# Performance work log

Measured on AMD Instinct MI355X. Metric: run time of the kernel, lower is better.

## Reference

```python
import jax, jax.numpy as jnp
import numpy as np

THETA = 10000.0
D_K = 128
MAX_SEQ_LEN = 4096
BATCH = 32
SEQ = 4096


def _build_rot(theta, d_k, max_seq_len):
    """Precompute the [max_seq_len, d_k, d_k] block-diagonal 2x2 rotation stack,
    matching the torch module's buffer construction."""
    ks = 2.0 * jnp.arange(d_k // 2, dtype=jnp.float32)
    inv_theta = 1.0 / (theta ** (ks / d_k))                      # [d_k/2]
    pos = jnp.arange(max_seq_len, dtype=jnp.float32)
    ang = pos[:, None] * inv_theta[None, :]                      # [S, d_k/2]
    c, s = jnp.cos(ang), jnp.sin(ang)
    ev = jnp.arange(0, d_k, 2)
    od = ev + 1
    rot = jnp.zeros((max_seq_len, d_k, d_k), dtype=jnp.float32)
    rot = (rot.at[:, ev, ev].set(c)
              .at[:, od, od].set(c)
              .at[:, ev, od].set(-s)
              .at[:, od, ev].set(s))
    return rot


def setup_inputs() -> dict:
    key = jax.random.key(0)
    k1, k2 = jax.random.split(key)
    x = jax.random.normal(k1, (BATCH, SEQ, D_K), dtype=jnp.float32)
    token_positions = jax.random.randint(k2, (BATCH, SEQ), 0, MAX_SEQ_LEN)
    rot = _build_rot(THETA, D_K, MAX_SEQ_LEN)                    # [S, d_k, d_k] buffer
    return {"x": x, "token_positions": token_positions, "rot": rot}


def reference(x, token_positions, rot):
    # The torch forward OVERWRITES token_positions with arange(min_seq_len).
    min_seq_len = min(x.shape[-2], token_positions.shape[-1])
    pos = jnp.arange(min_seq_len)
    # Dense block-diagonal rotation matmul per position (faithful to the module's einsum).
    # rot[pos]: [S, d_k, d_k], x: [B, S, d_k] -> [B, S, d_k]
    return jnp.einsum('sij,bsj->bsi', rot[pos], x)
```

## Files before the change

### kernel.cpp

```cpp
#include <hip/hip_runtime.h>


#define ROPE_DK    128
#define ROPE_HALF  64
#define ROPE_SEQ   4096
#define ROPE_BATCH 32

#define LOG2_THETA 13.287712379549449f

__global__ void rope_build_table(float* __restrict__ tbl) {
    int t = blockIdx.x * blockDim.x + threadIdx.x;
    if (t >= ROPE_SEQ * ROPE_HALF) return;
    int s = t >> 6;
    int k = t & 63;
    float ex  = (float)(2 * k) * (1.0f / (float)ROPE_DK);
    float inv = exp2f(-ex * LOG2_THETA);
    float ang = (float)s * inv;
    float sn, cs;
    sincosf(ang, &sn, &cs);
    reinterpret_cast<float2*>(tbl)[t] = make_float2(cs, sn);
}

__global__ void rope_apply(const float4* __restrict__ x,
                           const float4* __restrict__ tbl,
                           float4* __restrict__ out, int n4) {
    int idx    = blockIdx.x * blockDim.x + threadIdx.x;
    int stride = gridDim.x * blockDim.x;
    for (; idx < n4; idx += stride) {
        float4 t = tbl[idx & (ROPE_SEQ * 32 - 1)];
        float4 v = x[idx];
        float4 o;
        o.x = t.x * v.x - t.y * v.y;
        o.y = t.y * v.x + t.x * v.y;
        o.z = t.z * v.z - t.w * v.w;
        o.w = t.w * v.z + t.z * v.w;
        out[idx] = o;
    }
}

__global__ void rope_fused(const float4* __restrict__ x,
                           float4* __restrict__ out, int n4) {
    int idx    = blockIdx.x * blockDim.x + threadIdx.x;
    int stride = gridDim.x * blockDim.x;
    for (; idx < n4; idx += stride) {
        int sd = idx & (ROPE_SEQ * 32 - 1);
        int s  = sd >> 5;
        int d4 = sd & 31;
        float4 v = x[idx];
        float4 o;
        #pragma unroll
        for (int half = 0; half < 2; ++half) {
            int k = 2 * d4 + half;
            float ex  = (float)(2 * k) * (1.0f / (float)ROPE_DK);
            float inv = exp2f(-ex * LOG2_THETA);
            float ang = (float)s * inv;
            float sn, cs;
            sincosf(ang, &sn, &cs);
            if (half == 0) { o.x = cs * v.x - sn * v.y; o.y = sn * v.x + cs * v.y; }
            else           { o.z = cs * v.z - sn * v.w; o.w = sn * v.z + cs * v.w; }
        }
        out[idx] = o;
    }
}

extern "C" void kernel_launch(void* const* d_in, const int* in_sizes, int n_in,
                              void* d_out, int out_size, void* d_ws, size_t ws_size,
                              hipStream_t stream) {
    const float* x = (const float*)d_in[0];
    float* out = (float*)d_out;

    const int n4 = ROPE_BATCH * ROPE_SEQ * (ROPE_DK / 4);
    const size_t tbl_bytes = (size_t)ROPE_SEQ * ROPE_DK * sizeof(float);

    if (ws_size >= tbl_bytes) {
        float* tbl = (float*)d_ws;
        int nt = ROPE_SEQ * ROPE_HALF;
        rope_build_table<<<(nt + 255) / 256, 256, 0, stream>>>(tbl);
        rope_apply<<<2048, 256, 0, stream>>>((const float4*)x, (const float4*)tbl,
                                             (float4*)out, n4);
    } else {
        rope_fused<<<2048, 256, 0, stream>>>((const float4*)x, (float4*)out, n4);
    }
}
```

Before: 353.6 us.

## Fuse RoPE into single kernel with loop-invariant hoisted sincos and nontemporal IO

Removes the separate table-building kernel and workspace table reads. The kernel computes the rotation angles once per thread, before the grid-stride loop, because the stride is a multiple of the sequence-row period so each thread's position and dim never change. Loads and stores use nontemporal hints to stream data. Correctness depends on the fixed grid size keeping the stride aligned to the row period.

After: 346.2 us. 1.02x faster.

```diff
diff --git a/kernel.cpp b/kernel.cpp
--- a/kernel.cpp
+++ b/kernel.cpp
@@ -1,84 +1,48 @@
 #include <hip/hip_runtime.h>
 
 
+typedef float f32x4 __attribute__((ext_vector_type(4)));
+
 #define ROPE_DK    128
-#define ROPE_HALF  64
 #define ROPE_SEQ   4096
 #define ROPE_BATCH 32
-
 #define LOG2_THETA 13.287712379549449f
 
-__global__ void rope_build_table(float* __restrict__ tbl) {
-    int t = blockIdx.x * blockDim.x + threadIdx.x;
-    if (t >= ROPE_SEQ * ROPE_HALF) return;
-    int s = t >> 6;
-    int k = t & 63;
-    float ex  = (float)(2 * k) * (1.0f / (float)ROPE_DK);
-    float inv = exp2f(-ex * LOG2_THETA);
-    float ang = (float)s * inv;
-    float sn, cs;
-    sincosf(ang, &sn, &cs);
-    reinterpret_cast<float2*>(tbl)[t] = make_float2(cs, sn);
-}
+__global__ __launch_bounds__(256) void rope_fused(const f32x4* __restrict__ x,
+                                                  f32x4* __restrict__ out) {
+    constexpr int n4   = ROPE_BATCH * ROPE_SEQ * (ROPE_DK / 4);
+    constexpr int rowm = ROPE_SEQ * 32 - 1;
+    const int tid    = blockIdx.x * 256 + threadIdx.x;
+    const int stride = gridDim.x * 256;
 
-__global__ void rope_apply(const float4* __restrict__ x,
-                           const float4* __restrict__ tbl,
-                           float4* __restrict__ out, int n4) {
-    int idx    = blockIdx.x * blockDim.x + threadIdx.x;
-    int stride = gridDim.x * blockDim.x;
-    for (; idx < n4; idx += stride) {
-        float4 t = tbl[idx & (ROPE_SEQ * 32 - 1)];
-        float4 v = x[idx];
-        float4 o;
-        o.x = t.x * v.x - t.y * v.y;
-        o.y = t.y * v.x + t.x * v.y;
-        o.z = t.z * v.z - t.w * v.w;
-        o.w = t.w * v.z + t.z * v.w;
-        out[idx] = o;
+    const int   sd  = tid & rowm;
+    const float pos = (float)(sd >> 5);
+    const int   d4  = sd & 31;
+    float sn0, cs0, sn1, cs1;
+    {
+        const float k0   = (float)(2 * d4);
+        const float k1   = k0 + 1.0f;
+        const float inv0 = exp2f(-(2.0f * k0) * (LOG2_THETA / 128.0f));
+        const float inv1 = exp2f(-(2.0f * k1) * (LOG2_THETA / 128.0f));
+        sincosf(pos * inv0, &sn0, &cs0);
+        sincosf(pos * inv1, &sn1, &cs1);
     }
-}
 
-__global__ void rope_fused(const float4* __restrict__ x,
-                           float4* __restrict__ out, int n4) {
-    int idx    = blockIdx.x * blockDim.x + threadIdx.x;
-    int stride = gridDim.x * blockDim.x;
-    for (; idx < n4; idx += stride) {
-        int sd = idx & (ROPE_SEQ * 32 - 1);
-        int s  = sd >> 5;
-        int d4 = sd & 31;
-        float4 v = x[idx];
-        float4 o;
-        #pragma unroll
-        for (int half = 0; half < 2; ++half) {
-            int k = 2 * d4 + half;
-            float ex  = (float)(2 * k) * (1.0f / (float)ROPE_DK);
-            float inv = exp2f(-ex * LOG2_THETA);
-            float ang = (float)s * inv;
-            float sn, cs;
-            sincosf(ang, &sn, &cs);
-            if (half == 0) { o.x = cs * v.x - sn * v.y; o.y = sn * v.x + cs * v.y; }
-            else           { o.z = cs * v.z - sn * v.w; o.w = sn * v.z + cs * v.w; }
-        }
-        out[idx] = o;
+    for (int idx = tid; idx < n4; idx += stride) {
+        f32x4 v = __builtin_nontemporal_load(&x[idx]);
+        f32x4 o;
+        o.x = cs0 * v.x - sn0 * v.y;
+        o.y = sn0 * v.x + cs0 * v.y;
+        o.z = cs1 * v.z - sn1 * v.w;
+        o.w = sn1 * v.z + cs1 * v.w;
+        __builtin_nontemporal_store(o, &out[idx]);
     }
 }
 
 extern "C" void kernel_launch(void* const* d_in, const int* in_sizes, int n_in,
                               void* d_out, int out_size, void* d_ws, size_t ws_size,
                               hipStream_t stream) {
-    const float* x = (const float*)d_in[0];
-    float* out = (float*)d_out;
-
-    const int n4 = ROPE_BATCH * ROPE_SEQ * (ROPE_DK / 4);
-    const size_t tbl_bytes = (size_t)ROPE_SEQ * ROPE_DK * sizeof(float);
-
-    if (ws_size >= tbl_bytes) {
-        float* tbl = (float*)d_ws;
-        int nt = ROPE_SEQ * ROPE_HALF;
-        rope_build_table<<<(nt + 255) / 256, 256, 0, stream>>>(tbl);
-        rope_apply<<<2048, 256, 0, stream>>>((const float4*)x, (const float4*)tbl,
-                                             (float4*)out, n4);
-    } else {
-        rope_fused<<<2048, 256, 0, stream>>>((const float4*)x, (float4*)out, n4);
-    }
+    const f32x4* x   = (const f32x4*)d_in[0];
+    f32x4*       out = (f32x4*)d_out;
+    rope_fused<<<2048, 256, 0, stream>>>(x, out);
 }
```
